# Kernel optimization log

Hardware: AMD Instinct MI355X
Metric: run time of the kernel (lower is better)

## Reference

```python
import jax, jax.numpy as jnp
import numpy as np

EPS = 1e-5

def binarize(x):
    # det Binarize: sign with zeros mapped to +1
    return jnp.where(x >= 0, 1.0, -1.0).astype(x.dtype)

def conv3x3(x, w, stride=1):
    return jax.lax.conv_general_dilated(
        x, w, window_strides=(stride, stride), padding=((1, 1), (1, 1)),
        dimension_numbers=('NCHW', 'OIHW', 'NCHW'))

def batchnorm_train(x, gamma, beta):
    # training-mode BN: biased batch stats over (N, H, W)
    mean = jnp.mean(x, axis=(0, 2, 3), keepdims=True)
    var = jnp.mean(jnp.square(x - mean), axis=(0, 2, 3), keepdims=True)
    xn = (x - mean) * jax.lax.rsqrt(var + EPS)
    return xn * gamma[None, :, None, None] + beta[None, :, None, None]

def setup_inputs() -> dict:
    key = jax.random.key(0)
    k1, k2, k3 = jax.random.split(key, 3)
    C = 256
    return {
        'x': jax.random.normal(k1, (64, C, 28, 28), dtype=jnp.float32),
        'w1': jax.random.normal(k2, (C, C, 3, 3), dtype=jnp.float32) * 0.05,
        'w2': jax.random.normal(k3, (C, C, 3, 3), dtype=jnp.float32) * 0.05,
        'gamma1': jnp.ones((C,), jnp.float32),
        'beta1': jnp.zeros((C,), jnp.float32),
        'gamma2': jnp.ones((C,), jnp.float32),
        'beta2': jnp.zeros((C,), jnp.float32),
    }

def reference(x, w1, w2, gamma1, beta1, gamma2, beta2):
    residual = x
    # conv1: binarized activations and weights, 3x3 pad=1 stride=1
    out = conv3x3(binarize(x), binarize(w1))
    out = batchnorm_train(out, gamma1, beta1)
    out = jnp.clip(out, -1.0, 1.0)  # Hardtanh
    # conv2
    out = conv3x3(binarize(out), binarize(w2))
    out = out + residual
    # do_bntan
    out = batchnorm_train(out, gamma2, beta2)
    out = jnp.clip(out, -1.0, 1.0)
    return out
```

## Files before the change

kernel.cpp:

```cpp
#include <hip/hip_runtime.h>
#include <stdint.h>

typedef int v4i __attribute__((ext_vector_type(4)));

constexpr int C     = 256;
constexpr int H     = 28, W = 28;
constexpr int HW    = H * W;
constexpr int NB    = 64;
constexpr int GP    = NB * HW;
constexpr int CNT   = GP;
constexpr int TOTAL = NB * C * HW;
constexpr int MT    = 112;
constexpr int NBLK  = GP / MT;
constexpr int LROWS = 176;
constexpr int ZROW  = LROWS * 16;


#define SB(f) ((f) < 0.f ? 0xFF : 0x01)

#define XPE(e, pw0, pw1, pw2, pw3, sh) { \
    const float4 v = *(const float4*)(base + (size_t)(e) * HW); \
    pw0 |= SB(v.x) << (sh); pw1 |= SB(v.y) << (sh); \
    pw2 |= SB(v.z) << (sh); pw3 |= SB(v.w) << (sh); }

__global__ void pack_all_kernel(const float* __restrict__ pw1, const float* __restrict__ pw2,
                                const float* __restrict__ x,
                                v4i* __restrict__ wbf1, v4i* __restrict__ wbf2,
                                v4i* __restrict__ xb, double* __restrict__ stats) {
    __shared__ signed char sgn[36864];
    const int t = threadIdx.x;
    const int bid = blockIdx.x;
    if (bid < 32) {
        const int g = bid & 15;
        const float* w = (bid >> 4) ? pw2 : pw1;
        v4i* dst       = (bid >> 4) ? wbf2 : wbf1;
        const float4* wg = (const float4*)(w + (size_t)g * 16 * 2304);
        int* sg4 = (int*)sgn;
        for (int pass = 0; pass < 36; ++pass) {
            const int m4 = pass * 256 + t;
            float4 v = wg[m4];
            int pk = SB(v.x) | (SB(v.y) << 8) | (SB(v.z) << 16) | (SB(v.w) << 24);
            sg4[m4] = pk;
        }
        __syncthreads();
        const int l = t & 63, kb = t >> 6;
        const int colb = (l & 15) * 2304;
        const int cib  = kb * 64 + (l >> 4) * 16;
        for (int tp = 0; tp < 9; ++tp) {
            int b0 = 0, b1 = 0, b2 = 0, b3 = 0;
#pragma unroll
            for (int e = 0; e < 16; ++e) {
                int b = (int)(unsigned char)sgn[colb + (cib + e) * 9 + tp];
                int sh = (e & 3) * 8;
                if (e < 4) b0 |= b << sh; else if (e < 8) b1 |= b << sh;
                else if (e < 12) b2 |= b << sh; else b3 |= b << sh;
            }
            v4i o; o.x = b0; o.y = b1; o.z = b2; o.w = b3;
            dst[((tp * 4 + kb) * 16 + g) * 64 + l] = o;
        }
    } else {
        const int local = bid - 32;
        const int ch = local / 49;
        const int i4 = (local % 49) * 256 + t;
        if (ch == 0 && i4 < 1024) stats[i4] = 0.0;
        const int gp = i4 * 4;
        const int n = gp / HW, p = gp % HW;
        const float* base = x + (size_t)n * C * HW + (size_t)(ch * 16) * HW + p;
        int a0=0,a1=0,a2=0,a3=0;
        int b0=0,b1=0,b2=0,b3=0;
        int c0=0,c1=0,c2=0,c3=0;
        int d0=0,d1=0,d2=0,d3=0;
        XPE( 0,a0,b0,c0,d0, 0) XPE( 1,a0,b0,c0,d0, 8) XPE( 2,a0,b0,c0,d0,16) XPE( 3,a0,b0,c0,d0,24)
        XPE( 4,a1,b1,c1,d1, 0) XPE( 5,a1,b1,c1,d1, 8) XPE( 6,a1,b1,c1,d1,16) XPE( 7,a1,b1,c1,d1,24)
        XPE( 8,a2,b2,c2,d2, 0) XPE( 9,a2,b2,c2,d2, 8) XPE(10,a2,b2,c2,d2,16) XPE(11,a2,b2,c2,d2,24)
        XPE(12,a3,b3,c3,d3, 0) XPE(13,a3,b3,c3,d3, 8) XPE(14,a3,b3,c3,d3,16) XPE(15,a3,b3,c3,d3,24)
        v4i* dst = xb + (size_t)ch * GP + gp;
        v4i o0; o0.x=a0; o0.y=a1; o0.z=a2; o0.w=a3; dst[0] = o0;
        v4i o1; o1.x=b0; o1.y=b1; o1.z=b2; o1.w=b3; dst[1] = o1;
        v4i o2; o2.x=c0; o2.y=c1; o2.z=c2; o2.w=c3; dst[2] = o2;
        v4i o3; o3.x=d0; o3.y=d1; o3.z=d2; o3.w=d3; dst[3] = o3;
    }
}

__global__ void finalize_kernel(const double* __restrict__ sum,
                                const double* __restrict__ sumsq,
                                const float* __restrict__ gamma,
                                const float* __restrict__ beta,
                                float* __restrict__ scale,
                                float* __restrict__ shift) {
    int c = threadIdx.x;
    double mean = sum[c] / (double)CNT;
    double var  = sumsq[c] / (double)CNT - mean * mean;
    double inv  = 1.0 / sqrt(var + 1e-5);
    scale[c] = (float)inv * gamma[c];
    shift[c] = beta[c] - (float)(mean * inv) * gamma[c];
}

typedef short short4v __attribute__((ext_vector_type(4)));

#define SPE(e, pw0, pw1, pw2, pw3, sh) { \
    const short4v v = *(const short4v*)(base + (size_t)(e) * HW); \
    const float sc = s_scale[chb + (e)], sf = s_shift[chb + (e)]; \
    pw0 |= SB((float)v.x * sc + sf) << (sh); pw1 |= SB((float)v.y * sc + sf) << (sh); \
    pw2 |= SB((float)v.z * sc + sf) << (sh); pw3 |= SB((float)v.w * sc + sf) << (sh); }

__global__ void bn_signpack_kernel(const short* __restrict__ y,
                                   const float* __restrict__ scale,
                                   const float* __restrict__ shift,
                                   v4i* __restrict__ xb) {
    __shared__ float s_scale[C], s_shift[C];
    const int t = threadIdx.x;
    s_scale[t] = scale[t]; s_shift[t] = shift[t];
    __syncthreads();
    const int local = blockIdx.x;
    const int ch = local / 49;
    const int i4 = (local % 49) * 256 + t;
    const int gp = i4 * 4;
    const int n = gp / HW, p = gp % HW;
    const short* base = y + (size_t)n * C * HW + (size_t)(ch * 16) * HW + p;
    const int chb = ch * 16;
    int a0=0,a1=0,a2=0,a3=0;
    int b0=0,b1=0,b2=0,b3=0;
    int c0=0,c1=0,c2=0,c3=0;
    int d0=0,d1=0,d2=0,d3=0;
    SPE( 0,a0,b0,c0,d0, 0) SPE( 1,a0,b0,c0,d0, 8) SPE( 2,a0,b0,c0,d0,16) SPE( 3,a0,b0,c0,d0,24)
    SPE( 4,a1,b1,c1,d1, 0) SPE( 5,a1,b1,c1,d1, 8) SPE( 6,a1,b1,c1,d1,16) SPE( 7,a1,b1,c1,d1,24)
    SPE( 8,a2,b2,c2,d2, 0) SPE( 9,a2,b2,c2,d2, 8) SPE(10,a2,b2,c2,d2,16) SPE(11,a2,b2,c2,d2,24)
    SPE(12,a3,b3,c3,d3, 0) SPE(13,a3,b3,c3,d3, 8) SPE(14,a3,b3,c3,d3,16) SPE(15,a3,b3,c3,d3,24)
    v4i* dst = xb + (size_t)ch * GP + gp;
    v4i o0; o0.x=a0; o0.y=a1; o0.z=a2; o0.w=a3; dst[0] = o0;
    v4i o1; o1.x=b0; o1.y=b1; o1.z=b2; o1.w=b3; dst[1] = o1;
    v4i o2; o2.x=c0; o2.y=c1; o2.z=c2; o2.w=c3; dst[2] = o2;
    v4i o3; o3.x=d0; o3.y=d1; o3.z=d2; o3.w=d3; dst[3] = o3;
}


#define ACCD(m) v4i c##m##_0={0,0,0,0}, c##m##_1={0,0,0,0}, \
                    c##m##_2={0,0,0,0}, c##m##_3={0,0,0,0};
#define ACC_DECL ACCD(0) ACCD(1) ACCD(2) ACCD(3) ACCD(4) ACCD(5) ACCD(6)

#define MFMA(a,b,c) c = __builtin_amdgcn_mfma_i32_16x16x64_i8(a, b, c, 0, 0, 0);

#define B_LOADQ(P, idx) { const v4i* bp = wbf + (idx); \
    P##0 = bp[0]; P##1 = bp[64]; P##2 = bp[128]; P##3 = bp[192]; }

#define ARD(P, m, cb) P##m = xl[R##m + ((cb) ^ S##m)];
#define ARDALL(P, cb) ARD(P,0,cb) ARD(P,1,cb) ARD(P,2,cb) ARD(P,3,cb) \
                      ARD(P,4,cb) ARD(P,5,cb) ARD(P,6,cb)

#define MFMAG(A,B,g) MFMA(A##0,B##g,c0_##g) MFMA(A##1,B##g,c1_##g) MFMA(A##2,B##g,c2_##g) \
                     MFMA(A##3,B##g,c3_##g) MFMA(A##4,B##g,c4_##g) MFMA(A##5,B##g,c5_##g) \
                     MFMA(A##6,B##g,c6_##g)
#define MFMA_C(A,B) __builtin_amdgcn_s_setprio(1); \
    MFMAG(A,B,0) MFMAG(A,B,1) MFMAG(A,B,2) MFMAG(A,B,3) \
    __builtin_amdgcn_s_setprio(0);

#define TV1(m) { const bool mk = ((unsigned)(cm##m + dc) < 28u) && \
                                 ((unsigned)(rm##m + dr) < 28u); \
    R##m = mk ? (lrb + 16 * (m)) * 16 : ZROW; S##m = mk ? sm : 0; }
#define TAPVARS(TPX) { const int dr = (TPX)/3 - 1, dc = (TPX)%3 - 1; \
    const int lrb = 32 + llo + dr * W + dc; const int sm = lrb & 15; \
    TV1(0) TV1(1) TV1(2) TV1(3) TV1(4) TV1(5) TV1(6) }

#define PMV(m) const int gx##m = gp0 + (m)*16 + llo; \
    const int pmv##m = gx##m % HW; \
    const int rm##m = pmv##m / W, cm##m = pmv##m % W;

#define EPIV(m,g) { \
    const int gpv = gp0 + (m)*16 + lhi*4; \
    const int nn = gpv / HW; const int pp = gpv - nn*HW; \
    const size_t base = (size_t)nn*(C*HW) + (size_t)(wn*64+(g)*16+llo)*HW + pp; \
    const v4i cc = c##m##_##g; \
    if constexpr (HAS_RES) { \
        const float4 r = *(const float4*)(residual + base); \
        float4 o; o.x = (float)cc.x + r.x; o.y = (float)cc.y + r.y; \
        o.z = (float)cc.z + r.z; o.w = (float)cc.w + r.w; \
        *(float4*)((float*)yout + base) = o; \
        sy##g += o.x + o.y + o.z + o.w; \
        sq##g += o.x*o.x + o.y*o.y + o.z*o.z + o.w*o.w; \
    } else { \
        int2 o; o.x = (cc.x & 0xFFFF) | (cc.y << 16); \
        o.y = (cc.z & 0xFFFF) | (cc.w << 16); \
        *(int2*)((short*)yout + base) = o; \
        const float fx = (float)cc.x, fy = (float)cc.y, fz = (float)cc.z, fw = (float)cc.w; \
        sy##g += fx + fy + fz + fw; \
        sq##g += fx*fx + fy*fy + fz*fz + fw*fw; \
    } }
#define EPIM(m) EPIV(m,0) EPIV(m,1) EPIV(m,2) EPIV(m,3)

#define REDN(g) { float s1 = sy##g, s2 = sq##g; \
    s1 += __shfl_down(s1, 32); s1 += __shfl_down(s1, 16); \
    s2 += __shfl_down(s2, 32); s2 += __shfl_down(s2, 16); \
    if (l < 16) { const int co = wn*64 + (g)*16 + l; \
        atomicAdd(&sum[co], (double)s1); atomicAdd(&sumsq[co], (double)s2); } }

template<bool HAS_RES, typename OUT_T>
__launch_bounds__(256, 2)
__global__ void bconv_mfma(const v4i* __restrict__ xb,
                           const v4i* __restrict__ wbf,
                           const float* __restrict__ residual,
                           OUT_T* __restrict__ yout,
                           double* __restrict__ sum, double* __restrict__ sumsq) {
    __shared__ v4i xl[LROWS * 16 + 16];
    const int t   = threadIdx.x;
    const int gp0 = blockIdx.x * MT;

    for (int pass = 0; pass < 11; ++pass) {
        const int i = pass * 256 + t;
        const int c = i / LROWS;
        const int r = i - c * LROWS;
        int gsrc = min(max(gp0 - 32 + r, 0), GP - 1);
        xl[r * 16 + (c ^ (r & 15))] = xb[(size_t)c * GP + gsrc];
    }
    if (t < 16) { v4i z = {0,0,0,0}; xl[ZROW + t] = z; }
    __syncthreads();

    const int l = t & 63, wn = t >> 6;
    const int llo = l & 15, lhi = l >> 4;

    PMV(0) PMV(1) PMV(2) PMV(3) PMV(4) PMV(5) PMV(6)

    ACC_DECL
    const int bw = wn * 256 + l;

    int R0,R1,R2,R3,R4,R5,R6, S0,S1,S2,S3,S4,S5,S6;
    TAPVARS(0)
    v4i bP0,bP1,bP2,bP3, bQ0,bQ1,bQ2,bQ3;
    v4i aP0,aP1,aP2,aP3,aP4,aP5,aP6, aQ0,aQ1,aQ2,aQ3,aQ4,aQ5,aQ6;
    B_LOADQ(bP, bw)
    ARDALL(aP, lhi)

#pragma unroll 1
    for (int tp = 0; tp < 9; ++tp) {
        const int tb = bw + tp * 4096;
        B_LOADQ(bQ, tb + 1024)
        ARDALL(aQ, 4 + lhi)
        MFMA_C(aP, bP)
        B_LOADQ(bP, tb + 2048)
        ARDALL(aP, 8 + lhi)
        MFMA_C(aQ, bQ)
        B_LOADQ(bQ, tb + 3072)
        ARDALL(aQ, 12 + lhi)
        MFMA_C(aP, bP)
        const int tpn = (tp < 8) ? tp + 1 : 8;
        TAPVARS(tpn)
        B_LOADQ(bP, bw + tpn * 4096)
        ARDALL(aP, lhi)
        MFMA_C(aQ, bQ)
    }

    float sy0 = 0, sy1 = 0, sy2 = 0, sy3 = 0;
    float sq0 = 0, sq1 = 0, sq2 = 0, sq3 = 0;
    EPIM(0) EPIM(1) EPIM(2) EPIM(3) EPIM(4) EPIM(5) EPIM(6)
    REDN(0) REDN(1) REDN(2) REDN(3)
}

__global__ void bn_clip_kernel(const float4* __restrict__ z,
                               const float* __restrict__ scale,
                               const float* __restrict__ shift,
                               float4* __restrict__ out) {
    __shared__ float s_scale[C], s_shift[C];
    const int t = threadIdx.x;
    s_scale[t] = scale[t]; s_shift[t] = shift[t];
    __syncthreads();
    for (int i = blockIdx.x * blockDim.x + t; i < TOTAL / 4;
         i += gridDim.x * blockDim.x) {
        int c = (i / (HW / 4)) & (C - 1);
        float s = s_scale[c], b = s_shift[c];
        float4 v = z[i];
        v.x = fminf(1.f, fmaxf(-1.f, v.x * s + b));
        v.y = fminf(1.f, fmaxf(-1.f, v.y * s + b));
        v.z = fminf(1.f, fmaxf(-1.f, v.z * s + b));
        v.w = fminf(1.f, fmaxf(-1.f, v.w * s + b));
        out[i] = v;
    }
}

extern "C" void kernel_launch(void* const* d_in, const int* in_sizes, int n_in,
                              void* d_out, int out_size, void* d_ws, size_t ws_size,
                              hipStream_t stream) {
    const float* x  = (const float*)d_in[0];
    const float* w1 = (const float*)d_in[1];
    const float* w2 = (const float*)d_in[2];
    const float* g1 = (const float*)d_in[3];
    const float* b1 = (const float*)d_in[4];
    const float* g2 = (const float*)d_in[5];
    const float* b2 = (const float*)d_in[6];
    float* out = (float*)d_out;

    char* ws = (char*)d_ws;
    size_t off = 0;
    float* z2 = (float*)(ws + off);   off += (size_t)TOTAL * 4;
    v4i* xb1  = (v4i*)(ws + off);     off += (size_t)GP * 16 * 16;
    v4i* xb2  = (v4i*)(ws + off);     off += (size_t)GP * 16 * 16;
    v4i* wbf1 = (v4i*)(ws + off);     off += (size_t)36864 * 16;
    v4i* wbf2 = (v4i*)(ws + off);     off += (size_t)36864 * 16;
    double* stats = (double*)(ws + off); off += 4 * 256 * 8;
    double* sum1 = stats, *sumsq1 = stats + 256, *sum2 = stats + 512, *sumsq2 = stats + 768;
    float* coefs = (float*)(ws + off);   off += 4 * 256 * 4;
    float* scale1 = coefs, *shift1 = coefs + 256, *scale2 = coefs + 512, *shift2 = coefs + 768;

    short* y1 = (short*)d_out;

    pack_all_kernel<<<32 + 784, 256, 0, stream>>>(w1, w2, x, wbf1, wbf2, xb1, stats);

    bconv_mfma<false, short><<<NBLK, 256, 0, stream>>>(xb1, wbf1, nullptr, y1, sum1, sumsq1);
    finalize_kernel<<<1, 256, 0, stream>>>(sum1, sumsq1, g1, b1, scale1, shift1);
    bn_signpack_kernel<<<784, 256, 0, stream>>>(y1, scale1, shift1, xb2);
    bconv_mfma<true, float><<<NBLK, 256, 0, stream>>>(xb2, wbf2, x, z2, sum2, sumsq2);
    finalize_kernel<<<1, 256, 0, stream>>>(sum2, sumsq2, g2, b2, scale2, shift2);
    bn_clip_kernel<<<4096, 256, 0, stream>>>((const float4*)z2, scale2, shift2, (float4*)out);
}
```

Baseline: 215.5 us.

## Switch binary conv to 32x32x32 int8 MFMA tiles and fold BN finalize into consumers

```diff
diff --git a/kernel.cpp b/kernel.cpp
--- a/kernel.cpp
+++ b/kernel.cpp
@@ -1,7 +1,8 @@
 #include <hip/hip_runtime.h>
 #include <stdint.h>
 
-typedef int v4i __attribute__((ext_vector_type(4)));
+typedef int v4i  __attribute__((ext_vector_type(4)));
+typedef int v16i __attribute__((ext_vector_type(16)));
 
 constexpr int C     = 256;
 constexpr int H     = 28, W = 28;
@@ -10,9 +11,9 @@
 constexpr int GP    = NB * HW;
 constexpr int CNT   = GP;
 constexpr int TOTAL = NB * C * HW;
-constexpr int MT    = 112;
+constexpr int MT    = 128;
 constexpr int NBLK  = GP / MT;
-constexpr int LROWS = 176;
+constexpr int LROWS = 192;
 constexpr int ZROW  = LROWS * 16;
 
 
@@ -31,10 +32,10 @@
     const int t = threadIdx.x;
     const int bid = blockIdx.x;
     if (bid < 32) {
-        const int g = bid & 15;
+        const int cg = bid & 15;
         const float* w = (bid >> 4) ? pw2 : pw1;
         v4i* dst       = (bid >> 4) ? wbf2 : wbf1;
-        const float4* wg = (const float4*)(w + (size_t)g * 16 * 2304);
+        const float4* wg = (const float4*)(w + (size_t)cg * 16 * 2304);
         int* sg4 = (int*)sgn;
         for (int pass = 0; pass < 36; ++pass) {
             const int m4 = pass * 256 + t;
@@ -43,20 +44,23 @@
             sg4[m4] = pk;
         }
         __syncthreads();
-        const int l = t & 63, kb = t >> 6;
-        const int colb = (l & 15) * 2304;
-        const int cib  = kb * 64 + (l >> 4) * 16;
+        const int co_l = t & 15;
+        const int lh   = (t >> 4) & 1;
+        const int ks   = t >> 5;
+        const int g    = cg >> 1, h = cg & 1;
+        const int lane = h * 16 + co_l + lh * 32;
+        const int ci0  = ks * 32 + lh * 16;
         for (int tp = 0; tp < 9; ++tp) {
             int b0 = 0, b1 = 0, b2 = 0, b3 = 0;
 #pragma unroll
             for (int e = 0; e < 16; ++e) {
-                int b = (int)(unsigned char)sgn[colb + (cib + e) * 9 + tp];
+                int b = (int)(unsigned char)sgn[co_l * 2304 + (ci0 + e) * 9 + tp];
                 int sh = (e & 3) * 8;
                 if (e < 4) b0 |= b << sh; else if (e < 8) b1 |= b << sh;
                 else if (e < 12) b2 |= b << sh; else b3 |= b << sh;
             }
             v4i o; o.x = b0; o.y = b1; o.z = b2; o.w = b3;
-            dst[((tp * 4 + kb) * 16 + g) * 64 + l] = o;
+            dst[((tp * 8 + ks) * 8 + g) * 64 + lane] = o;
         }
     } else {
         const int local = bid - 32;
@@ -82,18 +86,17 @@
     }
 }
 
-__global__ void finalize_kernel(const double* __restrict__ sum,
-                                const double* __restrict__ sumsq,
-                                const float* __restrict__ gamma,
-                                const float* __restrict__ beta,
-                                float* __restrict__ scale,
-                                float* __restrict__ shift) {
-    int c = threadIdx.x;
-    double mean = sum[c] / (double)CNT;
-    double var  = sumsq[c] / (double)CNT - mean * mean;
+__device__ __forceinline__ void finalize_coefs(int t, const double* __restrict__ sum,
+                                               const double* __restrict__ sumsq,
+                                               const float* __restrict__ gamma,
+                                               const float* __restrict__ beta,
+                                               float* __restrict__ s_scale,
+                                               float* __restrict__ s_shift) {
+    double mean = sum[t] / (double)CNT;
+    double var  = sumsq[t] / (double)CNT - mean * mean;
     double inv  = 1.0 / sqrt(var + 1e-5);
-    scale[c] = (float)inv * gamma[c];
-    shift[c] = beta[c] - (float)(mean * inv) * gamma[c];
+    s_scale[t] = (float)inv * gamma[t];
+    s_shift[t] = beta[t] - (float)(mean * inv) * gamma[t];
 }
 
 typedef short short4v __attribute__((ext_vector_type(4)));
@@ -105,12 +108,14 @@
     pw2 |= SB((float)v.z * sc + sf) << (sh); pw3 |= SB((float)v.w * sc + sf) << (sh); }
 
 __global__ void bn_signpack_kernel(const short* __restrict__ y,
-                                   const float* __restrict__ scale,
-                                   const float* __restrict__ shift,
+                                   const double* __restrict__ sum,
+                                   const double* __restrict__ sumsq,
+                                   const float* __restrict__ gamma,
+                                   const float* __restrict__ beta,
                                    v4i* __restrict__ xb) {
     __shared__ float s_scale[C], s_shift[C];
     const int t = threadIdx.x;
-    s_scale[t] = scale[t]; s_shift[t] = shift[t];
+    finalize_coefs(t, sum, sumsq, gamma, beta, s_scale, s_shift);
     __syncthreads();
     const int local = blockIdx.x;
     const int ch = local / 49;
@@ -135,63 +140,64 @@
 }
 
 
-#define ACCD(m) v4i c##m##_0={0,0,0,0}, c##m##_1={0,0,0,0}, \
-                    c##m##_2={0,0,0,0}, c##m##_3={0,0,0,0};
-#define ACC_DECL ACCD(0) ACCD(1) ACCD(2) ACCD(3) ACCD(4) ACCD(5) ACCD(6)
-
-#define MFMA(a,b,c) c = __builtin_amdgcn_mfma_i32_16x16x64_i8(a, b, c, 0, 0, 0);
-
-#define B_LOADQ(P, idx) { const v4i* bp = wbf + (idx); \
-    P##0 = bp[0]; P##1 = bp[64]; P##2 = bp[128]; P##3 = bp[192]; }
-
-#define ARD(P, m, cb) P##m = xl[R##m + ((cb) ^ S##m)];
-#define ARDALL(P, cb) ARD(P,0,cb) ARD(P,1,cb) ARD(P,2,cb) ARD(P,3,cb) \
-                      ARD(P,4,cb) ARD(P,5,cb) ARD(P,6,cb)
-
-#define MFMAG(A,B,g) MFMA(A##0,B##g,c0_##g) MFMA(A##1,B##g,c1_##g) MFMA(A##2,B##g,c2_##g) \
-                     MFMA(A##3,B##g,c3_##g) MFMA(A##4,B##g,c4_##g) MFMA(A##5,B##g,c5_##g) \
-                     MFMA(A##6,B##g,c6_##g)
-#define MFMA_C(A,B) __builtin_amdgcn_s_setprio(1); \
-    MFMAG(A,B,0) MFMAG(A,B,1) MFMAG(A,B,2) MFMAG(A,B,3) \
+#define Z16 {0,0,0,0,0,0,0,0,0,0,0,0,0,0,0,0}
+#define ACC_DECL v16i c00=Z16,c10=Z16,c20=Z16,c30=Z16, \
+                      c01=Z16,c11=Z16,c21=Z16,c31=Z16;
+
+#define MFMA32(a,b,c) c = __builtin_amdgcn_mfma_i32_32x32x32_i8(a, b, c, 0, 0, 0);
+
+#define B_LOAD2(P, kidx) { const v4i* bp = wbf + (kidx) + bwl; \
+    P##0 = bp[0]; P##1 = bp[64]; }
+
+#define A_READ4(P, cb) { \
+    P##0 = xl[R0 + ((cb) ^ S0)]; P##1 = xl[R1 + ((cb) ^ S1)]; \
+    P##2 = xl[R2 + ((cb) ^ S2)]; P##3 = xl[R3 + ((cb) ^ S3)]; }
+
+#define MFMA_C8(A,B) __builtin_amdgcn_s_setprio(1); \
+    MFMA32(A##0,B##0,c00) MFMA32(A##1,B##0,c10) MFMA32(A##2,B##0,c20) MFMA32(A##3,B##0,c30) \
+    MFMA32(A##0,B##1,c01) MFMA32(A##1,B##1,c11) MFMA32(A##2,B##1,c21) MFMA32(A##3,B##1,c31) \
     __builtin_amdgcn_s_setprio(0);
 
 #define TV1(m) { const bool mk = ((unsigned)(cm##m + dc) < 28u) && \
                                  ((unsigned)(rm##m + dr) < 28u); \
-    R##m = mk ? (lrb + 16 * (m)) * 16 : ZROW; S##m = mk ? sm : 0; }
+    const int r = 32 + l31 + 32 * (m) + doff; \
+    R##m = mk ? r * 16 : ZROW; S##m = mk ? (r & 15) : 0; }
 #define TAPVARS(TPX) { const int dr = (TPX)/3 - 1, dc = (TPX)%3 - 1; \
-    const int lrb = 32 + llo + dr * W + dc; const int sm = lrb & 15; \
-    TV1(0) TV1(1) TV1(2) TV1(3) TV1(4) TV1(5) TV1(6) }
-
-#define PMV(m) const int gx##m = gp0 + (m)*16 + llo; \
-    const int pmv##m = gx##m % HW; \
-    const int rm##m = pmv##m / W, cm##m = pmv##m % W;
-
-#define EPIV(m,g) { \
-    const int gpv = gp0 + (m)*16 + lhi*4; \
+    const int doff = dr * W + dc; \
+    TV1(0) TV1(1) TV1(2) TV1(3) }
+
+#define PMV(m) { const int gx = gp0 + (m)*32 + l31; \
+    const int pm = gx % HW; rm##m = pm / W; cm##m = pm % W; }
+
+#define EPIQ(m,gl,q) { \
+    const int gpv = gp0 + (m)*32 + (q)*8 + lh4; \
     const int nn = gpv / HW; const int pp = gpv - nn*HW; \
-    const size_t base = (size_t)nn*(C*HW) + (size_t)(wn*64+(g)*16+llo)*HW + pp; \
-    const v4i cc = c##m##_##g; \
+    const size_t base = (size_t)nn*(C*HW) + (size_t)(cob + (gl)*32) * HW + pp; \
     if constexpr (HAS_RES) { \
-        const float4 r = *(const float4*)(residual + base); \
-        float4 o; o.x = (float)cc.x + r.x; o.y = (float)cc.y + r.y; \
-        o.z = (float)cc.z + r.z; o.w = (float)cc.w + r.w; \
+        const float4 r4 = *(const float4*)(residual + base); \
+        float4 o; \
+        o.x = (float)(c##m##gl[(q)*4+0]) + r4.x; \
+        o.y = (float)(c##m##gl[(q)*4+1]) + r4.y; \
+        o.z = (float)(c##m##gl[(q)*4+2]) + r4.z; \
+        o.w = (float)(c##m##gl[(q)*4+3]) + r4.w; \
         *(float4*)((float*)yout + base) = o; \
-        sy##g += o.x + o.y + o.z + o.w; \
-        sq##g += o.x*o.x + o.y*o.y + o.z*o.z + o.w*o.w; \
+        sy##gl += o.x + o.y + o.z + o.w; \
+        sq##gl += o.x*o.x + o.y*o.y + o.z*o.z + o.w*o.w; \
     } else { \
-        int2 o; o.x = (cc.x & 0xFFFF) | (cc.y << 16); \
-        o.y = (cc.z & 0xFFFF) | (cc.w << 16); \
+        const int i0 = c##m##gl[(q)*4+0], i1 = c##m##gl[(q)*4+1]; \
+        const int i2 = c##m##gl[(q)*4+2], i3 = c##m##gl[(q)*4+3]; \
+        int2 o; o.x = (i0 & 0xFFFF) | (i1 << 16); o.y = (i2 & 0xFFFF) | (i3 << 16); \
         *(int2*)((short*)yout + base) = o; \
-        const float fx = (float)cc.x, fy = (float)cc.y, fz = (float)cc.z, fw = (float)cc.w; \
-        sy##g += fx + fy + fz + fw; \
-        sq##g += fx*fx + fy*fy + fz*fz + fw*fw; \
+        const float f0 = (float)i0, f1 = (float)i1, f2 = (float)i2, f3 = (float)i3; \
+        sy##gl += f0 + f1 + f2 + f3; \
+        sq##gl += f0*f0 + f1*f1 + f2*f2 + f3*f3; \
     } }
-#define EPIM(m) EPIV(m,0) EPIV(m,1) EPIV(m,2) EPIV(m,3)
-
-#define REDN(g) { float s1 = sy##g, s2 = sq##g; \
-    s1 += __shfl_down(s1, 32); s1 += __shfl_down(s1, 16); \
-    s2 += __shfl_down(s2, 32); s2 += __shfl_down(s2, 16); \
-    if (l < 16) { const int co = wn*64 + (g)*16 + l; \
+#define EPIM(m) EPIQ(m,0,0) EPIQ(m,0,1) EPIQ(m,0,2) EPIQ(m,0,3) \
+                EPIQ(m,1,0) EPIQ(m,1,1) EPIQ(m,1,2) EPIQ(m,1,3)
+
+#define RED32(gl) { float s1 = sy##gl, s2 = sq##gl; \
+    s1 += __shfl_down(s1, 32); s2 += __shfl_down(s2, 32); \
+    if (l < 32) { const int co = wn*64 + (gl)*32 + l; \
         atomicAdd(&sum[co], (double)s1); atomicAdd(&sumsq[co], (double)s2); } }
 
 template<bool HAS_RES, typename OUT_T>
@@ -205,7 +211,7 @@
     const int t   = threadIdx.x;
     const int gp0 = blockIdx.x * MT;
 
-    for (int pass = 0; pass < 11; ++pass) {
+    for (int pass = 0; pass < 12; ++pass) {
         const int i = pass * 256 + t;
         const int c = i / LROWS;
         const int r = i - c * LROWS;
@@ -216,52 +222,53 @@
     __syncthreads();
 
     const int l = t & 63, wn = t >> 6;
-    const int llo = l & 15, lhi = l >> 4;
-
-    PMV(0) PMV(1) PMV(2) PMV(3) PMV(4) PMV(5) PMV(6)
+    const int l31 = l & 31, lh = l >> 5, lh4 = lh * 4;
+
+    int rm0, cm0, rm1, cm1, rm2, cm2, rm3, cm3;
+    PMV(0) PMV(1) PMV(2) PMV(3)
 
     ACC_DECL
-    const int bw = wn * 256 + l;
-
-    int R0,R1,R2,R3,R4,R5,R6, S0,S1,S2,S3,S4,S5,S6;
+    const int bwl = wn * 128 + l;
+
+    int R0,R1,R2,R3, S0,S1,S2,S3;
     TAPVARS(0)
-    v4i bP0,bP1,bP2,bP3, bQ0,bQ1,bQ2,bQ3;
-    v4i aP0,aP1,aP2,aP3,aP4,aP5,aP6, aQ0,aQ1,aQ2,aQ3,aQ4,aQ5,aQ6;
-    B_LOADQ(bP, bw)
-    ARDALL(aP, lhi)
+    v4i bP0,bP1, bQ0,bQ1;
+    v4i aP0,aP1,aP2,aP3, aQ0,aQ1,aQ2,aQ3;
+    B_LOAD2(bP, 0)
+    A_READ4(aP, lh)
 
 #pragma unroll 1
     for (int tp = 0; tp < 9; ++tp) {
-        const int tb = bw + tp * 4096;
-        B_LOADQ(bQ, tb + 1024)
-        ARDALL(aQ, 4 + lhi)
-        MFMA_C(aP, bP)
-        B_LOADQ(bP, tb + 2048)
-        ARDALL(aP, 8 + lhi)
-        MFMA_C(aQ, bQ)
-        B_LOADQ(bQ, tb + 3072)
-        ARDALL(aQ, 12 + lhi)
-        MFMA_C(aP, bP)
+        const int tb = tp * 4096;
+        B_LOAD2(bQ, tb +  512) A_READ4(aQ,  2 + lh) MFMA_C8(aP, bP)
+        B_LOAD2(bP, tb + 1024) A_READ4(aP,  4 + lh) MFMA_C8(aQ, bQ)
+        B_LOAD2(bQ, tb + 1536) A_READ4(aQ,  6 + lh) MFMA_C8(aP, bP)
+        B_LOAD2(bP, tb + 2048) A_READ4(aP,  8 + lh) MFMA_C8(aQ, bQ)
+        B_LOAD2(bQ, tb + 2560) A_READ4(aQ, 10 + lh) MFMA_C8(aP, bP)
+        B_LOAD2(bP, tb + 3072) A_READ4(aP, 12 + lh) MFMA_C8(aQ, bQ)
+        B_LOAD2(bQ, tb + 3584) A_READ4(aQ, 14 + lh) MFMA_C8(aP, bP)
         const int tpn = (tp < 8) ? tp + 1 : 8;
         TAPVARS(tpn)
-        B_LOADQ(bP, bw + tpn * 4096)
-        ARDALL(aP, lhi)
-        MFMA_C(aQ, bQ)
+        B_LOAD2(bP, tpn * 4096)
+        A_READ4(aP, lh)
+        MFMA_C8(aQ, bQ)
     }
 
-    float sy0 = 0, sy1 = 0, sy2 = 0, sy3 = 0;
-    float sq0 = 0, sq1 = 0, sq2 = 0, sq3 = 0;
-    EPIM(0) EPIM(1) EPIM(2) EPIM(3) EPIM(4) EPIM(5) EPIM(6)
-    REDN(0) REDN(1) REDN(2) REDN(3)
+    float sy0 = 0, sy1 = 0, sq0 = 0, sq1 = 0;
+    const int cob = wn * 64 + l31;
+    EPIM(0) EPIM(1) EPIM(2) EPIM(3)
+    RED32(0) RED32(1)
 }
 
 __global__ void bn_clip_kernel(const float4* __restrict__ z,
-                               const float* __restrict__ scale,
-                               const float* __restrict__ shift,
+                               const double* __restrict__ sum,
+                               const double* __restrict__ sumsq,
+                               const float* __restrict__ gamma,
+                               const float* __restrict__ beta,
                                float4* __restrict__ out) {
     __shared__ float s_scale[C], s_shift[C];
     const int t = threadIdx.x;
-    s_scale[t] = scale[t]; s_shift[t] = shift[t];
+    finalize_coefs(t, sum, sumsq, gamma, beta, s_scale, s_shift);
     __syncthreads();
     for (int i = blockIdx.x * blockDim.x + t; i < TOTAL / 4;
          i += gridDim.x * blockDim.x) {
@@ -297,17 +304,14 @@
     v4i* wbf2 = (v4i*)(ws + off);     off += (size_t)36864 * 16;
     double* stats = (double*)(ws + off); off += 4 * 256 * 8;
     double* sum1 = stats, *sumsq1 = stats + 256, *sum2 = stats + 512, *sumsq2 = stats + 768;
-    float* coefs = (float*)(ws + off);   off += 4 * 256 * 4;
-    float* scale1 = coefs, *shift1 = coefs + 256, *scale2 = coefs + 512, *shift2 = coefs + 768;
 
     short* y1 = (short*)d_out;
 
     pack_all_kernel<<<32 + 784, 256, 0, stream>>>(w1, w2, x, wbf1, wbf2, xb1, stats);
 
     bconv_mfma<false, short><<<NBLK, 256, 0, stream>>>(xb1, wbf1, nullptr, y1, sum1, sumsq1);
-    finalize_kernel<<<1, 256, 0, stream>>>(sum1, sumsq1, g1, b1, scale1, shift1);
-    bn_signpack_kernel<<<784, 256, 0, stream>>>(y1, scale1, shift1, xb2);
+    bn_signpack_kernel<<<784, 256, 0, stream>>>(y1, sum1, sumsq1, g1, b1, xb2);
     bconv_mfma<true, float><<<NBLK, 256, 0, stream>>>(xb2, wbf2, x, z2, sum2, sumsq2);
-    finalize_kernel<<<1, 256, 0, stream>>>(sum2, sumsq2, g2, b2, scale2, shift2);
-    bn_clip_kernel<<<4096, 256, 0, stream>>>((const float4*)z2, scale2, shift2, (float4*)out);
-}
+    bn_clip_kernel<<<4096, 256, 0, stream>>>((const float4*)z2, sum2, sumsq2, g2, b2,
+                                             (float4*)out);
+}
```

Result: slower. 221.3 us (+2.7%).
